# Kernel tuning notes

Measured on AMD Instinct MI355X. Metric: run time of the kernel, lower is better.

## Reference

```python
import jax, jax.numpy as jnp
import numpy as np

N, NS, C = 100000, 16, 64
S = 8  # share_planes
EPS = 1e-5

def bn(x, g, b, m, v):
    # eval-mode BatchNorm1d over channel (last) axis
    return (x - m) * (g / jnp.sqrt(v + EPS)) + b

def setup_inputs() -> dict:
    key = jax.random.key(0)
    ks = jax.random.split(key, 24)
    d = {}
    d['p'] = jax.random.normal(ks[0], (N, 3), jnp.float32)
    d['x'] = jax.random.normal(ks[1], (N, C), jnp.float32)
    d['idx'] = jax.random.randint(ks[2], (N, NS), 0, N, jnp.int64)
    d['Wq'] = jax.random.normal(ks[3], (C, C), jnp.float32) * 0.1
    d['bq'] = jax.random.normal(ks[4], (C,), jnp.float32) * 0.1
    d['Wk'] = jax.random.normal(ks[5], (C, C), jnp.float32) * 0.1
    d['bk'] = jax.random.normal(ks[6], (C,), jnp.float32) * 0.1
    d['Wv'] = jax.random.normal(ks[7], (C, C), jnp.float32) * 0.1
    d['bv'] = jax.random.normal(ks[8], (C,), jnp.float32) * 0.1
    d['p_w1'] = jax.random.normal(ks[9], (3, 3), jnp.float32) * 0.5
    d['p_b1'] = jax.random.normal(ks[10], (3,), jnp.float32) * 0.1
    d['p_bn_g'] = jax.random.normal(ks[11], (3,), jnp.float32)
    d['p_bn_b'] = jax.random.normal(ks[12], (3,), jnp.float32) * 0.1
    d['p_bn_m'] = jnp.zeros((3,), jnp.float32)
    d['p_bn_v'] = jnp.ones((3,), jnp.float32)
    d['p_w2'] = jax.random.normal(ks[13], (C, 3), jnp.float32) * 0.3
    d['p_b2'] = jax.random.normal(ks[14], (C,), jnp.float32) * 0.1
    d['w_bn1_g'] = jax.random.normal(ks[15], (C,), jnp.float32)
    d['w_bn1_b'] = jax.random.normal(ks[16], (C,), jnp.float32) * 0.1
    d['w_bn1_m'] = jnp.zeros((C,), jnp.float32)
    d['w_bn1_v'] = jnp.ones((C,), jnp.float32)
    d['w_w1'] = jax.random.normal(ks[17], (C // S, C), jnp.float32) * 0.1
    d['w_b1'] = jax.random.normal(ks[18], (C // S,), jnp.float32) * 0.1
    d['w_bn2_g'] = jax.random.normal(ks[19], (C // S,), jnp.float32)
    d['w_bn2_b'] = jax.random.normal(ks[20], (C // S,), jnp.float32) * 0.1
    d['w_bn2_m'] = jnp.zeros((C // S,), jnp.float32)
    d['w_bn2_v'] = jnp.ones((C // S,), jnp.float32)
    d['w_w2'] = jax.random.normal(ks[21], (C // S, C // S), jnp.float32) * 0.3
    d['w_b2'] = jax.random.normal(ks[22], (C // S,), jnp.float32) * 0.1
    return d

def reference(p, x, idx, Wq, bq, Wk, bk, Wv, bv,
              p_w1, p_b1, p_bn_g, p_bn_b, p_bn_m, p_bn_v, p_w2, p_b2,
              w_bn1_g, w_bn1_b, w_bn1_m, w_bn1_v, w_w1, w_b1,
              w_bn2_g, w_bn2_b, w_bn2_m, w_bn2_v, w_w2, w_b2):
    n, ns = idx.shape
    c = Wv.shape[0]
    s = S
    # q/k/v projections
    x_q = x @ Wq.T + bq                       # (n, c)
    x_k = (x @ Wk.T + bk)[idx]                # (n, ns, c) gather
    x_v = (x @ Wv.T + bv)[idx]                # (n, ns, c) gather
    # relative positions of boundary-KNN neighbors
    p_r = p[idx] - p[:, None, :]              # (n, ns, 3)
    # linear_p: Linear(3,3) -> BN(3) -> ReLU -> Linear(3,c)
    p_r = p_r @ p_w1.T + p_b1
    p_r = jax.nn.relu(bn(p_r, p_bn_g, p_bn_b, p_bn_m, p_bn_v))
    p_r = p_r @ p_w2.T + p_b2                 # (n, ns, c)
    # attention logits (out_planes // mid_planes == 1, so sum(2) is identity)
    w = x_k - x_q[:, None, :] + p_r
    # linear_w: BN(c) -> ReLU -> Linear(c, c/s) -> BN(c/s) -> ReLU -> Linear(c/s, c/s)
    w = jax.nn.relu(bn(w, w_bn1_g, w_bn1_b, w_bn1_m, w_bn1_v))
    w = w @ w_w1.T + w_b1                     # (n, ns, c/s)
    w = jax.nn.relu(bn(w, w_bn2_g, w_bn2_b, w_bn2_m, w_bn2_v))
    w = w @ w_w2.T + w_b2                     # (n, ns, c/s)
    w = jax.nn.softmax(w, axis=1)             # softmax over neighbors
    # grouped weighted reduce with shared attention weights
    out = ((x_v + p_r).reshape(n, ns, s, c // s) * w[:, :, None, :]).sum(1)
    return out.reshape(n, c)
```

## Files before the change

kernel.cpp:

```cpp
#include <hip/hip_runtime.h>
#include <hip/hip_bf16.h>

typedef unsigned short u16;
typedef unsigned int   u32;
typedef __attribute__((ext_vector_type(8))) short bf16x8;
typedef __attribute__((ext_vector_type(4))) float f32x4;

#define EPSV 1e-5f

__device__ __forceinline__ float b2f(u16 u) {
    union { u32 i; float f; } x; x.i = ((u32)u) << 16; return x.f;
}
__device__ __forceinline__ u16 f2b(float f) {
    union { float f; u32 i; } x; x.f = f;
    u32 lsb = (x.i >> 16) & 1u;
    return (u16)((x.i + 0x7fffu + lsb) >> 16);
}
__device__ __forceinline__ bf16x8 pack8(float4 a, float4 b) {
    bf16x8 r;
    r[0] = (short)f2b(a.x); r[1] = (short)f2b(a.y);
    r[2] = (short)f2b(a.z); r[3] = (short)f2b(a.w);
    r[4] = (short)f2b(b.x); r[5] = (short)f2b(b.y);
    r[6] = (short)f2b(b.z); r[7] = (short)f2b(b.w);
    return r;
}
__device__ __forceinline__ float rdlane_f(float v, int lane) {
    return __uint_as_float(__builtin_amdgcn_readlane(__float_as_uint(v), lane));
}

__global__ __launch_bounds__(256) void kvq_mfma(
    const float* __restrict__ x,
    const float* __restrict__ Wq, const float* __restrict__ bq,
    const float* __restrict__ Wk, const float* __restrict__ bk,
    const float* __restrict__ Wv, const float* __restrict__ bv,
    u16* __restrict__ qb, u32* __restrict__ kvb,
    int N)
{
    __shared__ u16 Wl[3 * 64 * 72];
    __shared__ u16 xl[64 * 72];
    const int t = threadIdx.x;

    const float* Wg[3] = {Wq, Wk, Wv};
#pragma unroll
    for (int mat = 0; mat < 3; ++mat) {
        const float4* Wsrc = (const float4*)Wg[mat];
#pragma unroll
        for (int it = 0; it < 4; ++it) {
            int id4 = t + it * 256;
            int row = id4 >> 4;
            int c4  = id4 & 15;
            float4 f = Wsrc[id4];
            u32 lo = (u32)f2b(f.x) | ((u32)f2b(f.y) << 16);
            u32 hi = (u32)f2b(f.z) | ((u32)f2b(f.w) << 16);
            u32* d = (u32*)&Wl[(mat * 64 + row) * 72 + c4 * 4];
            d[0] = lo; d[1] = hi;
        }
    }
    int base = blockIdx.x * 64;
#pragma unroll
    for (int it = 0; it < 4; ++it) {
        int id4 = t + it * 256;
        int row = id4 >> 4;
        int c4  = id4 & 15;
        int gi = base + row; if (gi >= N) gi = N - 1;
        float4 f = ((const float4*)(x + (size_t)gi * 64))[c4];
        u32 lo = (u32)f2b(f.x) | ((u32)f2b(f.y) << 16);
        u32 hi = (u32)f2b(f.z) | ((u32)f2b(f.w) << 16);
        u32* d = (u32*)&xl[row * 72 + c4 * 4];
        d[0] = lo; d[1] = hi;
    }
    __syncthreads();

    const int lane = t & 63;
    const int wid  = t >> 6;
    const int n_   = lane & 15;
    const int quad = lane >> 4;

    bf16x8 a0 = *(const bf16x8*)&xl[(wid * 16 + n_) * 72 + quad * 8];
    bf16x8 a1 = *(const bf16x8*)&xl[(wid * 16 + n_) * 72 + 32 + quad * 8];

    f32x4 acc[12];
#pragma unroll
    for (int nt = 0; nt < 12; ++nt) {
        int mat = nt >> 2;
        int c = ((nt & 3) << 4) + n_;
        bf16x8 b0 = *(const bf16x8*)&Wl[(mat * 64 + c) * 72 + quad * 8];
        bf16x8 b1 = *(const bf16x8*)&Wl[(mat * 64 + c) * 72 + 32 + quad * 8];
        f32x4 z = {0.f, 0.f, 0.f, 0.f};
        z = __builtin_amdgcn_mfma_f32_16x16x32_bf16(a0, b0, z, 0, 0, 0);
        z = __builtin_amdgcn_mfma_f32_16x16x32_bf16(a1, b1, z, 0, 0, 0);
        acc[nt] = z;
    }

    int rbase = base + wid * 16 + quad * 4;
#pragma unroll
    for (int g4 = 0; g4 < 4; ++g4) {
        int c = (g4 << 4) + n_;
        float biasq = bq[c], biask = bk[c], biasv = bv[c];
#pragma unroll
        for (int r = 0; r < 4; ++r) {
            int i2 = rbase + r;
            if (i2 < N) {
                qb[(size_t)i2 * 64 + c] = f2b(acc[g4][r] + biasq);
                u32 kvp = (u32)f2b(acc[4 + g4][r] + biask)
                        | ((u32)f2b(acc[8 + g4][r] + biasv) << 16);
                kvb[(size_t)i2 * 64 + c] = kvp;
            }
        }
    }
}

__global__ __launch_bounds__(256) void attn_mfma(
    const float* __restrict__ p, const int* __restrict__ idx32,
    const u16* __restrict__ qb, const u32* __restrict__ kvb,
    const float* __restrict__ pw1, const float* __restrict__ pb1,
    const float* __restrict__ g3, const float* __restrict__ b3,
    const float* __restrict__ m3, const float* __restrict__ v3,
    const float* __restrict__ pw2, const float* __restrict__ pb2,
    const float* __restrict__ g1, const float* __restrict__ b1,
    const float* __restrict__ m1, const float* __restrict__ v1,
    const float* __restrict__ ww1, const float* __restrict__ wb1,
    const float* __restrict__ g2, const float* __restrict__ b2c,
    const float* __restrict__ m2, const float* __restrict__ v2,
    const float* __restrict__ ww2, const float* __restrict__ wb2,
    float* __restrict__ out, int N)
{
    __shared__ u16   wrT[4][16 * 72];
    __shared__ u16   hbnT[4][16 * 16];
    __shared__ float wT[4][16 * 9];

    const int lane = threadIdx.x & 63;
    const int wid  = threadIdx.x >> 6;
    int i = blockIdx.x * 4 + wid;
    bool active = (i < N);
    int ic = active ? i : 0;
    const int m    = lane & 7;
    const int n16  = lane & 15;
    const int quad = lane >> 4;

    bool idx64 = (idx32[1] == 0) & (idx32[3] == 0) & (idx32[5] == 0) & (idx32[7] == 0);

    float qc  = b2f(qb[(size_t)ic * 64 + lane]);
    float s1  = g1[lane] * rsqrtf(v1[lane] + EPSV);
    float bb1 = b1[lane] - m1[lane] * s1;
    float pw2_0 = pw2[lane * 3 + 0];
    float pw2_1 = pw2[lane * 3 + 1];
    float pw2_2 = pw2[lane * 3 + 2];
    float pb2c  = pb2[lane];
    float s2   = g2[m] * rsqrtf(v2[m] + EPSV);
    float bb2v = b2c[m] - m2[m] * s2;
    float wb1m = wb1[m];
    float wb2m = wb2[m];
    float pix = p[(size_t)ic * 3 + 0];
    float piy = p[(size_t)ic * 3 + 1];
    float piz = p[(size_t)ic * 3 + 2];

    size_t ii = (size_t)ic * 16 + n16;
    int nbr = idx64 ? idx32[ii * 2] : idx32[ii];
    if ((unsigned)nbr >= (unsigned)N) nbr = 0;

    float u0l, u1l, u2l;
    {
        float pdx = p[(size_t)nbr * 3 + 0] - pix;
        float pdy = p[(size_t)nbr * 3 + 1] - piy;
        float pdz = p[(size_t)nbr * 3 + 2] - piz;
        float a0 = pw1[0] * pdx + pw1[1] * pdy + pw1[2] * pdz + pb1[0];
        float a1 = pw1[3] * pdx + pw1[4] * pdy + pw1[5] * pdz + pb1[1];
        float a2 = pw1[6] * pdx + pw1[7] * pdy + pw1[8] * pdz + pb1[2];
        float sa0 = g3[0] * rsqrtf(v3[0] + EPSV);
        float sa1 = g3[1] * rsqrtf(v3[1] + EPSV);
        float sa2 = g3[2] * rsqrtf(v3[2] + EPSV);
        u0l = fmaxf(0.f, a0 * sa0 + (b3[0] - m3[0] * sa0));
        u1l = fmaxf(0.f, a1 * sa1 + (b3[1] - m3[1] * sa1));
        u2l = fmaxf(0.f, a2 * sa2 + (b3[2] - m3[2] * sa2));
    }

    bf16x8 b0, b1f;
    {
        const float4* r4 = (const float4*)(ww1 + (size_t)m * 64);
        b0  = pack8(r4[quad * 2 + 0], r4[quad * 2 + 1]);
        b1f = pack8(r4[8 + quad * 2 + 0], r4[8 + quad * 2 + 1]);
    }
    bf16x8 b2f_ = {};
    if (quad == 0) {
        const float4* r4 = (const float4*)(ww2 + (size_t)m * 8);
        b2f_ = pack8(r4[0], r4[1]);
    }

    u32 kvw[16];
#pragma unroll
    for (int j = 0; j < 16; ++j) {
        int nj = __builtin_amdgcn_readlane(nbr, j);
        kvw[j] = kvb[(size_t)nj * 64 + lane];
    }

    float vpr[16];
    u16* myWr = wrT[wid];
#pragma unroll
    for (int j = 0; j < 16; ++j) {
        float u0 = rdlane_f(u0l, j);
        float u1 = rdlane_f(u1l, j);
        float u2 = rdlane_f(u2l, j);
        float pr = fmaf(u0, pw2_0, fmaf(u1, pw2_1, fmaf(u2, pw2_2, pb2c)));
        u32 w = kvw[j];
        float kc = __uint_as_float(w << 16);
        float vc = __uint_as_float(w & 0xffff0000u);
        vpr[j] = vc + pr;
        float wr = fmaxf(0.f, (kc - qc + pr) * s1 + bb1);
        myWr[j * 72 + lane] = f2b(wr);
    }
    asm volatile("s_waitcnt lgkmcnt(0)" ::: "memory");
    __builtin_amdgcn_sched_barrier(0);

    bf16x8 a0 = *(const bf16x8*)&myWr[n16 * 72 + quad * 8];
    bf16x8 a1 = *(const bf16x8*)&myWr[n16 * 72 + 32 + quad * 8];
    f32x4 h1 = {0.f, 0.f, 0.f, 0.f};
    h1 = __builtin_amdgcn_mfma_f32_16x16x32_bf16(a0, b0,  h1, 0, 0, 0);
    h1 = __builtin_amdgcn_mfma_f32_16x16x32_bf16(a1, b1f, h1, 0, 0, 0);

    u16* myH = hbnT[wid];
#pragma unroll
    for (int r = 0; r < 4; ++r) {
        float hb = fmaxf(0.f, (h1[r] + wb1m) * s2 + bb2v);
        myH[(quad * 4 + r) * 16 + m] = f2b(hb);
    }
    asm volatile("s_waitcnt lgkmcnt(0)" ::: "memory");
    __builtin_amdgcn_sched_barrier(0);

    bf16x8 a2 = {};
    if (quad == 0) a2 = *(const bf16x8*)&myH[n16 * 16];
    f32x4 scd = {0.f, 0.f, 0.f, 0.f};
    scd = __builtin_amdgcn_mfma_f32_16x16x32_bf16(a2, b2f_, scd, 0, 0, 0);

    float e[4];
    float mx = -1e30f;
#pragma unroll
    for (int r = 0; r < 4; ++r) { e[r] = scd[r] + wb2m; mx = fmaxf(mx, e[r]); }
    mx = fmaxf(mx, __shfl_xor(mx, 16, 64));
    mx = fmaxf(mx, __shfl_xor(mx, 32, 64));
    float s = 0.f;
#pragma unroll
    for (int r = 0; r < 4; ++r) { e[r] = __expf(e[r] - mx); s += e[r]; }
    s += __shfl_xor(s, 16, 64);
    s += __shfl_xor(s, 32, 64);
    float rs = 1.f / s;
    float* myW = wT[wid];
#pragma unroll
    for (int r = 0; r < 4; ++r) myW[(quad * 4 + r) * 9 + m] = e[r] * rs;
    asm volatile("s_waitcnt lgkmcnt(0)" ::: "memory");
    __builtin_amdgcn_sched_barrier(0);

    float acc = 0.f;
#pragma unroll
    for (int j = 0; j < 16; ++j) acc += myW[j * 9 + m] * vpr[j];
    if (active) out[(size_t)i * 64 + lane] = acc;
}

__global__ __launch_bounds__(256) void attn_fallback(
    const float* __restrict__ p, const int* __restrict__ idx32,
    const float* __restrict__ x,
    const float* __restrict__ Wq, const float* __restrict__ bq,
    const float* __restrict__ Wk, const float* __restrict__ bk,
    const float* __restrict__ Wv, const float* __restrict__ bv,
    const float* __restrict__ pw1, const float* __restrict__ pb1,
    const float* __restrict__ g3, const float* __restrict__ b3,
    const float* __restrict__ m3, const float* __restrict__ v3,
    const float* __restrict__ pw2, const float* __restrict__ pb2,
    const float* __restrict__ g1, const float* __restrict__ b1,
    const float* __restrict__ m1, const float* __restrict__ v1,
    const float* __restrict__ ww1, const float* __restrict__ wb1,
    const float* __restrict__ g2, const float* __restrict__ b2c,
    const float* __restrict__ m2, const float* __restrict__ v2,
    const float* __restrict__ ww2, const float* __restrict__ wb2,
    float* __restrict__ out, int N)
{
    const int lane = threadIdx.x & 63;
    const int wid  = threadIdx.x >> 6;
    int i = blockIdx.x * 4 + wid;
    bool active = (i < N);
    int ic = active ? i : 0;
    const int m = lane & 7;
    const int g = lane >> 3;
    bool idx64 = (idx32[1] == 0) & (idx32[3] == 0) & (idx32[5] == 0) & (idx32[7] == 0);

    float xi = x[(size_t)ic * 64 + lane];
    float qc = bq[lane];
#pragma unroll
    for (int kk = 0; kk < 64; ++kk)
        qc += __shfl(xi, kk, 64) * Wq[(size_t)lane * 64 + kk];
    float wkr[64], wvr[64];
#pragma unroll
    for (int tt = 0; tt < 64; ++tt) {
        wkr[tt] = Wk[(size_t)lane * 64 + tt];
        wvr[tt] = Wv[(size_t)lane * 64 + tt];
    }
    float bkc = bk[lane], bvc = bv[lane];
    float s1  = g1[lane] * rsqrtf(v1[lane] + EPSV);
    float bb1 = b1[lane] - m1[lane] * s1;
    float pw2_0 = pw2[lane * 3 + 0], pw2_1 = pw2[lane * 3 + 1], pw2_2 = pw2[lane * 3 + 2];
    float pb2c  = pb2[lane];
    float w1s[8];
#pragma unroll
    for (int tt = 0; tt < 8; ++tt) w1s[tt] = ww1[m * 64 + g * 8 + tt];
    float w2s[8];
#pragma unroll
    for (int tt = 0; tt < 8; ++tt) w2s[tt] = ww2[m * 8 + tt];
    float wb1m = wb1[m];
    float s2   = g2[m] * rsqrtf(v2[m] + EPSV);
    float bb2  = b2c[m] - m2[m] * s2;
    float wb2m = wb2[m];
    float pix = p[(size_t)ic * 3 + 0], piy = p[(size_t)ic * 3 + 1], piz = p[(size_t)ic * 3 + 2];
    size_t ii = (size_t)ic * 16 + (lane & 15);
    int nbr = idx64 ? idx32[ii * 2] : idx32[ii];
    if ((unsigned)nbr >= (unsigned)N) nbr = 0;
    float u0l, u1l, u2l;
    {
        float pdx = p[(size_t)nbr * 3 + 0] - pix;
        float pdy = p[(size_t)nbr * 3 + 1] - piy;
        float pdz = p[(size_t)nbr * 3 + 2] - piz;
        float a0 = pw1[0] * pdx + pw1[1] * pdy + pw1[2] * pdz + pb1[0];
        float a1 = pw1[3] * pdx + pw1[4] * pdy + pw1[5] * pdz + pb1[1];
        float a2 = pw1[6] * pdx + pw1[7] * pdy + pw1[8] * pdz + pb1[2];
        float sa0 = g3[0] * rsqrtf(v3[0] + EPSV);
        float sa1 = g3[1] * rsqrtf(v3[1] + EPSV);
        float sa2 = g3[2] * rsqrtf(v3[2] + EPSV);
        u0l = fmaxf(0.f, a0 * sa0 + (b3[0] - m3[0] * sa0));
        u1l = fmaxf(0.f, a1 * sa1 + (b3[1] - m3[1] * sa1));
        u2l = fmaxf(0.f, a2 * sa2 + (b3[2] - m3[2] * sa2));
    }
    float sc[16], vpr[16];
#pragma unroll
    for (int j = 0; j < 16; ++j) {
        int nj = __shfl(nbr, j, 64);
        float u0 = __shfl(u0l, j, 64);
        float u1 = __shfl(u1l, j, 64);
        float u2 = __shfl(u2l, j, 64);
        float pr = u0 * pw2_0 + u1 * pw2_1 + u2 * pw2_2 + pb2c;
        float xn = x[(size_t)nj * 64 + lane];
        float kc = bkc, vc = bvc;
#pragma unroll
        for (int kk = 0; kk < 64; ++kk) {
            float xk = __shfl(xn, kk, 64);
            kc += xk * wkr[kk];
            vc += xk * wvr[kk];
        }
        vpr[j] = vc + pr;
        float wr = fmaxf(0.f, (kc - qc + pr) * s1 + bb1);
        float partial = 0.f;
#pragma unroll
        for (int tt = 0; tt < 8; ++tt)
            partial += __shfl(wr, g * 8 + tt, 64) * w1s[tt];
        partial += __shfl_xor(partial, 8, 64);
        partial += __shfl_xor(partial, 16, 64);
        partial += __shfl_xor(partial, 32, 64);
        float hbn = fmaxf(0.f, (partial + wb1m) * s2 + bb2);
        float h2 = wb2m;
#pragma unroll
        for (int mm = 0; mm < 8; ++mm)
            h2 += __shfl(hbn, (lane & 56) | mm, 64) * w2s[mm];
        sc[j] = h2;
    }
    float mx = sc[0];
#pragma unroll
    for (int j = 1; j < 16; ++j) mx = fmaxf(mx, sc[j]);
    float sum = 0.f, acc = 0.f;
#pragma unroll
    for (int j = 0; j < 16; ++j) {
        float e = __expf(sc[j] - mx);
        sum += e;
        acc += e * vpr[j];
    }
    if (active) out[(size_t)i * 64 + lane] = acc / sum;
}

extern "C" void kernel_launch(void* const* d_in, const int* in_sizes, int n_in,
                              void* d_out, int out_size, void* d_ws, size_t ws_size,
                              hipStream_t stream) {
    const float* p   = (const float*)d_in[0];
    const float* x   = (const float*)d_in[1];
    const int* idx   = (const int*)d_in[2];
    const float* Wq  = (const float*)d_in[3];
    const float* bq  = (const float*)d_in[4];
    const float* Wk  = (const float*)d_in[5];
    const float* bk  = (const float*)d_in[6];
    const float* Wv  = (const float*)d_in[7];
    const float* bv  = (const float*)d_in[8];
    const float* pw1 = (const float*)d_in[9];
    const float* pb1 = (const float*)d_in[10];
    const float* g3  = (const float*)d_in[11];
    const float* b3  = (const float*)d_in[12];
    const float* m3  = (const float*)d_in[13];
    const float* v3  = (const float*)d_in[14];
    const float* pw2 = (const float*)d_in[15];
    const float* pb2 = (const float*)d_in[16];
    const float* g1  = (const float*)d_in[17];
    const float* b1  = (const float*)d_in[18];
    const float* m1  = (const float*)d_in[19];
    const float* v1  = (const float*)d_in[20];
    const float* ww1 = (const float*)d_in[21];
    const float* wb1 = (const float*)d_in[22];
    const float* g2  = (const float*)d_in[23];
    const float* b2  = (const float*)d_in[24];
    const float* m2  = (const float*)d_in[25];
    const float* v2  = (const float*)d_in[26];
    const float* ww2 = (const float*)d_in[27];
    const float* wb2 = (const float*)d_in[28];

    int N = in_sizes[0] / 3;
    size_t plane = (size_t)N * 64;
    bool tier1 = ws_size >= plane * 2 + plane * 4;

    u16* qb  = (u16*)d_ws;
    u32* kvb = (u32*)(qb + plane);

    int blocks = (N + 3) / 4;
    float* out = (float*)d_out;

    if (tier1) {
        int gblocks = (N + 63) / 64;
        kvq_mfma<<<gblocks, 256, 0, stream>>>(x, Wq, bq, Wk, bk, Wv, bv, qb, kvb, N);
        attn_mfma<<<blocks, 256, 0, stream>>>(p, idx, qb, kvb,
            pw1, pb1, g3, b3, m3, v3, pw2, pb2, g1, b1, m1, v1, ww1, wb1,
            g2, b2, m2, v2, ww2, wb2, out, N);
    } else {
        attn_fallback<<<blocks, 256, 0, stream>>>(p, idx, x, Wq, bq, Wk, bk, Wv, bv,
            pw1, pb1, g3, b3, m3, v3, pw2, pb2, g1, b1, m1, v1, ww1, wb1,
            g2, b2, m2, v2, ww2, wb2, out, N);
    }
}
```

Baseline: 240.0 us.

## Precompute folded BN/linear params and bf16 weights once; use packed bf16 converts

The first kernel's block 0 now folds the batch-norm scales and biases into fused per-channel constants, pre-folds the linear_p first layer, and converts ww1 and ww2 to bf16 in workspace. The attention kernel reads these instead of recomputing rsqrt and bf16 packing in every wave. It also uses v_cvt_pk_bf16_f32 for the conversions, folds q into the BN bias, and drops the wb2 bias, which cancels under the softmax over neighbours. The extra workspace requirement could push the fallback path if the workspace is exactly sized.

```diff
diff --git a/kernel.cpp b/kernel.cpp
--- a/kernel.cpp
+++ b/kernel.cpp
@@ -16,17 +16,15 @@
     u32 lsb = (x.i >> 16) & 1u;
     return (u16)((x.i + 0x7fffu + lsb) >> 16);
 }
-__device__ __forceinline__ bf16x8 pack8(float4 a, float4 b) {
-    bf16x8 r;
-    r[0] = (short)f2b(a.x); r[1] = (short)f2b(a.y);
-    r[2] = (short)f2b(a.z); r[3] = (short)f2b(a.w);
-    r[4] = (short)f2b(b.x); r[5] = (short)f2b(b.y);
-    r[6] = (short)f2b(b.z); r[7] = (short)f2b(b.w);
-    return r;
-}
 __device__ __forceinline__ float rdlane_f(float v, int lane) {
     return __uint_as_float(__builtin_amdgcn_readlane(__float_as_uint(v), lane));
 }
+__device__ __forceinline__ u32 cvtpk_bf16(float lo, float hi) {
+    u32 r;
+    asm("v_cvt_pk_bf16_f32 %0, %1, %2" : "=v"(r) : "v"(lo), "v"(hi));
+    return r;
+}
+
 
 __global__ __launch_bounds__(256) void kvq_mfma(
     const float* __restrict__ x,
@@ -34,6 +32,19 @@
     const float* __restrict__ Wk, const float* __restrict__ bk,
     const float* __restrict__ Wv, const float* __restrict__ bv,
     u16* __restrict__ qb, u32* __restrict__ kvb,
+    const float* __restrict__ g1, const float* __restrict__ b1,
+    const float* __restrict__ m1, const float* __restrict__ v1,
+    const float* __restrict__ pw2, const float* __restrict__ pb2,
+    const float* __restrict__ g2, const float* __restrict__ b2c,
+    const float* __restrict__ m2, const float* __restrict__ v2,
+    const float* __restrict__ wb1,
+    const float* __restrict__ pw1, const float* __restrict__ pb1,
+    const float* __restrict__ g3, const float* __restrict__ b3,
+    const float* __restrict__ m3, const float* __restrict__ v3,
+    const float* __restrict__ ww1, const float* __restrict__ ww2,
+    float4* __restrict__ chanP4, float2* __restrict__ chanP2,
+    float4* __restrict__ mP, float* __restrict__ pP,
+    u16* __restrict__ wwb1, u16* __restrict__ wwb2,
     int N)
 {
     __shared__ u16 Wl[3 * 64 * 72];
@@ -108,21 +119,41 @@
             }
         }
     }
+
+    if (blockIdx.x == 0) {
+        if (t < 64) {
+            float s1 = g1[t] * rsqrtf(v1[t] + EPSV);
+            float bb1 = b1[t] - m1[t] * s1;
+            chanP4[t] = make_float4(pw2[t * 3 + 0], pw2[t * 3 + 1], pw2[t * 3 + 2], pb2[t]);
+            chanP2[t] = make_float2(s1, bb1);
+            wwb2[t] = f2b(ww2[t]);
+        }
+        if (t < 8) {
+            float s2 = g2[t] * rsqrtf(v2[t] + EPSV);
+            float bb2f = b2c[t] - m2[t] * s2 + wb1[t] * s2;
+            mP[t] = make_float4(s2, bb2f, 0.f, 0.f);
+        }
+        if (t < 9) {
+            int r = t / 3;
+            float sa = g3[r] * rsqrtf(v3[r] + EPSV);
+            pP[t] = sa * pw1[t];
+        }
+        if (t >= 9 && t < 12) {
+            int r = t - 9;
+            float sa = g3[r] * rsqrtf(v3[r] + EPSV);
+            pP[t] = sa * (pb1[r] - m3[r]) + b3[r];
+        }
+        wwb1[t]       = f2b(ww1[t]);
+        wwb1[t + 256] = f2b(ww1[t + 256]);
+    }
 }
 
 __global__ __launch_bounds__(256) void attn_mfma(
     const float* __restrict__ p, const int* __restrict__ idx32,
     const u16* __restrict__ qb, const u32* __restrict__ kvb,
-    const float* __restrict__ pw1, const float* __restrict__ pb1,
-    const float* __restrict__ g3, const float* __restrict__ b3,
-    const float* __restrict__ m3, const float* __restrict__ v3,
-    const float* __restrict__ pw2, const float* __restrict__ pb2,
-    const float* __restrict__ g1, const float* __restrict__ b1,
-    const float* __restrict__ m1, const float* __restrict__ v1,
-    const float* __restrict__ ww1, const float* __restrict__ wb1,
-    const float* __restrict__ g2, const float* __restrict__ b2c,
-    const float* __restrict__ m2, const float* __restrict__ v2,
-    const float* __restrict__ ww2, const float* __restrict__ wb2,
+    const float4* __restrict__ chanP4, const float2* __restrict__ chanP2,
+    const float4* __restrict__ mP, const float* __restrict__ pP,
+    const u16* __restrict__ wwb1, const u16* __restrict__ wwb2,
     float* __restrict__ out, int N)
 {
     __shared__ u16   wrT[4][16 * 72];
@@ -140,17 +171,12 @@
 
     bool idx64 = (idx32[1] == 0) & (idx32[3] == 0) & (idx32[5] == 0) & (idx32[7] == 0);
 
+    float4 cp = chanP4[lane];
+    float2 sp = chanP2[lane];
+    float4 mp = mP[m];
     float qc  = b2f(qb[(size_t)ic * 64 + lane]);
-    float s1  = g1[lane] * rsqrtf(v1[lane] + EPSV);
-    float bb1 = b1[lane] - m1[lane] * s1;
-    float pw2_0 = pw2[lane * 3 + 0];
-    float pw2_1 = pw2[lane * 3 + 1];
-    float pw2_2 = pw2[lane * 3 + 2];
-    float pb2c  = pb2[lane];
-    float s2   = g2[m] * rsqrtf(v2[m] + EPSV);
-    float bb2v = b2c[m] - m2[m] * s2;
-    float wb1m = wb1[m];
-    float wb2m = wb2[m];
+    float s1  = sp.x;
+    float bb1q = sp.y - qc * s1;
     float pix = p[(size_t)ic * 3 + 0];
     float piy = p[(size_t)ic * 3 + 1];
     float piz = p[(size_t)ic * 3 + 2];
@@ -164,28 +190,15 @@
         float pdx = p[(size_t)nbr * 3 + 0] - pix;
         float pdy = p[(size_t)nbr * 3 + 1] - piy;
         float pdz = p[(size_t)nbr * 3 + 2] - piz;
-        float a0 = pw1[0] * pdx + pw1[1] * pdy + pw1[2] * pdz + pb1[0];
-        float a1 = pw1[3] * pdx + pw1[4] * pdy + pw1[5] * pdz + pb1[1];
-        float a2 = pw1[6] * pdx + pw1[7] * pdy + pw1[8] * pdz + pb1[2];
-        float sa0 = g3[0] * rsqrtf(v3[0] + EPSV);
-        float sa1 = g3[1] * rsqrtf(v3[1] + EPSV);
-        float sa2 = g3[2] * rsqrtf(v3[2] + EPSV);
-        u0l = fmaxf(0.f, a0 * sa0 + (b3[0] - m3[0] * sa0));
-        u1l = fmaxf(0.f, a1 * sa1 + (b3[1] - m3[1] * sa1));
-        u2l = fmaxf(0.f, a2 * sa2 + (b3[2] - m3[2] * sa2));
-    }
-
-    bf16x8 b0, b1f;
-    {
-        const float4* r4 = (const float4*)(ww1 + (size_t)m * 64);
-        b0  = pack8(r4[quad * 2 + 0], r4[quad * 2 + 1]);
-        b1f = pack8(r4[8 + quad * 2 + 0], r4[8 + quad * 2 + 1]);
-    }
+        u0l = fmaxf(0.f, fmaf(pP[0], pdx, fmaf(pP[1], pdy, fmaf(pP[2], pdz, pP[9]))));
+        u1l = fmaxf(0.f, fmaf(pP[3], pdx, fmaf(pP[4], pdy, fmaf(pP[5], pdz, pP[10]))));
+        u2l = fmaxf(0.f, fmaf(pP[6], pdx, fmaf(pP[7], pdy, fmaf(pP[8], pdz, pP[11]))));
+    }
+
+    bf16x8 b0  = *(const bf16x8*)&wwb1[(size_t)m * 64 + quad * 8];
+    bf16x8 b1f = *(const bf16x8*)&wwb1[(size_t)m * 64 + 32 + quad * 8];
     bf16x8 b2f_ = {};
-    if (quad == 0) {
-        const float4* r4 = (const float4*)(ww2 + (size_t)m * 8);
-        b2f_ = pack8(r4[0], r4[1]);
-    }
+    if (quad == 0) b2f_ = *(const bf16x8*)&wwb2[(size_t)m * 8];
 
     u32 kvw[16];
 #pragma unroll
@@ -197,17 +210,26 @@
     float vpr[16];
     u16* myWr = wrT[wid];
 #pragma unroll
-    for (int j = 0; j < 16; ++j) {
-        float u0 = rdlane_f(u0l, j);
-        float u1 = rdlane_f(u1l, j);
-        float u2 = rdlane_f(u2l, j);
-        float pr = fmaf(u0, pw2_0, fmaf(u1, pw2_1, fmaf(u2, pw2_2, pb2c)));
-        u32 w = kvw[j];
-        float kc = __uint_as_float(w << 16);
-        float vc = __uint_as_float(w & 0xffff0000u);
-        vpr[j] = vc + pr;
-        float wr = fmaxf(0.f, (kc - qc + pr) * s1 + bb1);
-        myWr[j * 72 + lane] = f2b(wr);
+    for (int jp = 0; jp < 8; ++jp) {
+        const int j0 = 2 * jp, j1 = j0 + 1;
+        float pr0 = fmaf(rdlane_f(u0l, j0), cp.x,
+                    fmaf(rdlane_f(u1l, j0), cp.y,
+                    fmaf(rdlane_f(u2l, j0), cp.z, cp.w)));
+        float pr1 = fmaf(rdlane_f(u0l, j1), cp.x,
+                    fmaf(rdlane_f(u1l, j1), cp.y,
+                    fmaf(rdlane_f(u2l, j1), cp.z, cp.w)));
+        u32 w0 = kvw[j0], w1 = kvw[j1];
+        float kc0 = __uint_as_float(w0 << 16);
+        float vc0 = __uint_as_float(w0 & 0xffff0000u);
+        float kc1 = __uint_as_float(w1 << 16);
+        float vc1 = __uint_as_float(w1 & 0xffff0000u);
+        vpr[j0] = vc0 + pr0;
+        vpr[j1] = vc1 + pr1;
+        float wr0 = fmaxf(0.f, fmaf(kc0 + pr0, s1, bb1q));
+        float wr1 = fmaxf(0.f, fmaf(kc1 + pr1, s1, bb1q));
+        u32 pk = cvtpk_bf16(wr0, wr1);
+        myWr[j0 * 72 + lane] = (u16)pk;
+        myWr[j1 * 72 + lane] = (u16)(pk >> 16);
     }
     asm volatile("s_waitcnt lgkmcnt(0)" ::: "memory");
     __builtin_amdgcn_sched_barrier(0);
@@ -219,10 +241,17 @@
     h1 = __builtin_amdgcn_mfma_f32_16x16x32_bf16(a1, b1f, h1, 0, 0, 0);
 
     u16* myH = hbnT[wid];
-#pragma unroll
-    for (int r = 0; r < 4; ++r) {
-        float hb = fmaxf(0.f, (h1[r] + wb1m) * s2 + bb2v);
-        myH[(quad * 4 + r) * 16 + m] = f2b(hb);
+    {
+        float hb0 = fmaxf(0.f, fmaf(h1[0], mp.x, mp.y));
+        float hb1 = fmaxf(0.f, fmaf(h1[1], mp.x, mp.y));
+        float hb2 = fmaxf(0.f, fmaf(h1[2], mp.x, mp.y));
+        float hb3 = fmaxf(0.f, fmaf(h1[3], mp.x, mp.y));
+        u32 pk01 = cvtpk_bf16(hb0, hb1);
+        u32 pk23 = cvtpk_bf16(hb2, hb3);
+        myH[(quad * 4 + 0) * 16 + m] = (u16)pk01;
+        myH[(quad * 4 + 1) * 16 + m] = (u16)(pk01 >> 16);
+        myH[(quad * 4 + 2) * 16 + m] = (u16)pk23;
+        myH[(quad * 4 + 3) * 16 + m] = (u16)(pk23 >> 16);
     }
     asm volatile("s_waitcnt lgkmcnt(0)" ::: "memory");
     __builtin_amdgcn_sched_barrier(0);
@@ -235,7 +264,7 @@
     float e[4];
     float mx = -1e30f;
 #pragma unroll
-    for (int r = 0; r < 4; ++r) { e[r] = scd[r] + wb2m; mx = fmaxf(mx, e[r]); }
+    for (int r = 0; r < 4; ++r) { e[r] = scd[r]; mx = fmaxf(mx, e[r]); }
     mx = fmaxf(mx, __shfl_xor(mx, 16, 64));
     mx = fmaxf(mx, __shfl_xor(mx, 32, 64));
     float s = 0.f;
@@ -408,20 +437,29 @@
 
     int N = in_sizes[0] / 3;
     size_t plane = (size_t)N * 64;
-    bool tier1 = ws_size >= plane * 2 + plane * 4;
+    bool tier1 = ws_size >= plane * 6 + 3072;
 
     u16* qb  = (u16*)d_ws;
     u32* kvb = (u32*)(qb + plane);
+    char* extra = (char*)d_ws + plane * 6;
+    float4* chanP4 = (float4*)(extra);
+    float2* chanP2 = (float2*)(extra + 1024);
+    float4* mP     = (float4*)(extra + 1536);
+    float*  pP     = (float*)(extra + 1664);
+    u16*    wwb1   = (u16*)(extra + 1792);
+    u16*    wwb2   = (u16*)(extra + 2816);
 
     int blocks = (N + 3) / 4;
     float* out = (float*)d_out;
 
     if (tier1) {
         int gblocks = (N + 63) / 64;
-        kvq_mfma<<<gblocks, 256, 0, stream>>>(x, Wq, bq, Wk, bk, Wv, bv, qb, kvb, N);
+        kvq_mfma<<<gblocks, 256, 0, stream>>>(x, Wq, bq, Wk, bk, Wv, bv, qb, kvb,
+            g1, b1, m1, v1, pw2, pb2, g2, b2, m2, v2, wb1,
+            pw1, pb1, g3, b3, m3, v3, ww1, ww2,
+            chanP4, chanP2, mP, pP, wwb1, wwb2, N);
         attn_mfma<<<blocks, 256, 0, stream>>>(p, idx, qb, kvb,
-            pw1, pb1, g3, b3, m3, v3, pw2, pb2, g1, b1, m1, v1, ww1, wb1,
-            g2, b2, m2, v2, ww2, wb2, out, N);
+            chanP4, chanP2, mP, pP, wwb1, wwb2, out, N);
     } else {
         attn_fallback<<<blocks, 256, 0, stream>>>(p, idx, x, Wq, bq, Wk, bk, Wv, bv,
             pw1, pb1, g3, b3, m3, v3, pw2, pb2, g1, b1, m1, v1, ww1, wb1,
```

New measurement: 210.0 us. 12.5% less time.
